# Kernel optimization log

Measured on AMD Instinct MI355X. Metric: run time of the kernel, lower is better.

The kernel has to match this reference:

```python
import jax, jax.numpy as jnp
import numpy as np

B, N, D_IN, D_OUT, NHOP = 16, 1024, 128, 128, 3


def setup_inputs() -> dict:
    key = jax.random.key(0)
    ks = jax.random.split(key, 7)
    x = jax.random.normal(ks[0], (B, N, D_IN), dtype=jnp.float32)
    # sparse-ish binary adjacency (float, as in the torch model) with self loops
    adj = (jax.random.uniform(ks[1], (B, N, N)) < 0.05).astype(jnp.float32)
    adj = jnp.maximum(adj, jnp.eye(N, dtype=jnp.float32)[None])
    # learned params (torch nn.Linear default-ish init scale)
    s_in = 1.0 / np.sqrt(D_IN)
    s_out = 1.0 / np.sqrt(2 * D_OUT)
    W_w = jax.random.uniform(ks[2], (D_OUT, D_IN), minval=-s_in, maxval=s_in, dtype=jnp.float32)
    W_b = jax.random.uniform(ks[3], (D_OUT,), minval=-s_in, maxval=s_in, dtype=jnp.float32)
    A = jax.random.normal(ks[4], (D_OUT, D_OUT), dtype=jnp.float32) * 0.02  # nn.Parameter(zeros) would kill signal; use small init
    gate_w = jax.random.uniform(ks[5], (1, 2 * D_OUT), minval=-s_out, maxval=s_out, dtype=jnp.float32)
    gate_b = jax.random.uniform(ks[6], (1,), minval=-s_out, maxval=s_out, dtype=jnp.float32)
    return {"x": x, "adj": adj, "W_w": W_w, "W_b": W_b, "A": A,
            "gate_w": gate_w, "gate_b": gate_b}


def reference(x, adj, W_w, W_b, A, gate_w, gate_b):
    # h = W(x): [B,N,D_OUT]
    h = jnp.einsum('bnd,od->bno', x, W_w) + W_b
    # bilinear score e[b,j,k] = (h A)_j . h_k, symmetrized
    e = jnp.einsum('bjl,bkl->bjk', jnp.einsum('bjd,de->bje', h, A), h)
    e = e + jnp.swapaxes(e, 1, 2)
    # masked softmax over dim=1 (as in the torch code), then re-mask
    att = jnp.where(adj > 0, e, jnp.zeros((), dtype=e.dtype))
    att = jax.nn.softmax(att, axis=1)
    att = att * adj
    retval = h
    for _ in range(NHOP):
        az = jax.nn.relu(jnp.einsum('bij,bjk->bik', att, retval))
        gate_in = jnp.concatenate([h, az], axis=-1)            # [B,N,2*D_OUT]
        coeff = jax.nn.sigmoid(jnp.einsum('bnf,of->bno', gate_in, gate_w) + gate_b)  # [B,N,1]
        retval = coeff * h + (1.0 - coeff) * az
    return retval
```

## Files before the change

kernel.cpp:

```cpp
#include <hip/hip_runtime.h>
#include <math.h>

#define Bn 16
#define Nn 1024
#define Dn 128

typedef unsigned short ushort;
typedef unsigned long long u64;
typedef short short8 __attribute__((ext_vector_type(8)));
typedef float f32x4 __attribute__((ext_vector_type(4)));
typedef ushort us8 __attribute__((ext_vector_type(8)));
typedef ushort us4 __attribute__((ext_vector_type(4)));

__device__ __forceinline__ ushort f2bf(float f) {
    unsigned u = __float_as_uint(f);
    u += 0x7fff + ((u >> 16) & 1);
    return (ushort)(u >> 16);
}
__device__ __forceinline__ float bf2f(ushort s) {
    return __uint_as_float(((unsigned)s) << 16);
}

#if defined(__has_builtin)
#if __has_builtin(__builtin_amdgcn_global_load_lds)
#define HAVE_GLL 1
#endif
#endif
#ifndef HAVE_GLL
#define HAVE_GLL 0
#endif

typedef __attribute__((address_space(1))) void as1_t;
typedef __attribute__((address_space(3))) void as3_t;

__device__ __forceinline__ void stage_group(const void* gbase, void* lbase, int lane) {
#if HAVE_GLL
    __builtin_amdgcn_global_load_lds((as1_t*)((const char*)gbase + lane * 16),
                                     (as3_t*)lbase, 16, 0, 0);
#else
    *(us8*)((char*)lbase + lane * 16) = *(const us8*)((const char*)gbase + lane * 16);
#endif
}


__global__ __launch_bounds__(256) void k_ph0(const float* __restrict__ Ww,
                                             const float* __restrict__ A,
                                             const float* __restrict__ adj,
                                             ushort* __restrict__ Whi, ushort* __restrict__ Wlo,
                                             ushort* __restrict__ Shi, ushort* __restrict__ Slo,
                                             float* __restrict__ Z, u64* __restrict__ bm) {
    int L = blockIdx.x, t = threadIdx.x;
    if (L < 64) {
        int i = L * 256 + t;
        float w = Ww[i];
        ushort wh = f2bf(w);
        Whi[i] = wh;
        Wlo[i] = f2bf(w - bf2f(wh));
        int e = i >> 7, d = i & 127;
        float s = A[i] + A[d * Dn + e];
        ushort sh = f2bf(s);
        Shi[i] = sh;
        Slo[i] = f2bf(s - bf2f(sh));
        Z[i] = (float)Nn;
    }
    int gwv = L * 4 + (t >> 6);
    int lane = t & 63;
    #pragma unroll 4
    for (int it = 0; it < 16; ++it) {
        int pair = gwv * 16 + it;
        const float* p = adj + (size_t)pair * 256 + lane * 4;
        float4 v = *(const float4*)p;
        u64 b0 = __ballot(v.x > 0.f);
        u64 b1 = __ballot(v.y > 0.f);
        u64 b2 = __ballot(v.z > 0.f);
        u64 b3 = __ballot(v.w > 0.f);
        if (lane == 0) {
            u64* d = bm + (size_t)pair * 4;
            d[0] = b0; d[1] = b1; d[2] = b2; d[3] = b3;
        }
    }
}

__global__ __launch_bounds__(256) void k_h(const float* __restrict__ x,
                                           const float* __restrict__ Wb,
                                           const ushort* __restrict__ Whi,
                                           const ushort* __restrict__ Wlo,
                                           const ushort* __restrict__ Shi,
                                           const ushort* __restrict__ Slo,
                                           float* __restrict__ h,
                                           ushort* __restrict__ h16f,
                                           ushort* __restrict__ g16f) {
    int I0 = blockIdx.x * 16;
    int t = threadIdx.x, w = t >> 6, lane = t & 63;
    int m = lane & 15, q = lane >> 4;

    __shared__ float xs[16][Dn + 4];
    __shared__ float hs[16][Dn + 4];
    __shared__ float gs_[16][Dn + 4];

    {
        int r = t >> 4, c8 = (t & 15) * 8;
        const float* src = x + (size_t)(I0 + r) * Dn + c8;
        *(float4*)&xs[r][c8]     = *(const float4*)(src);
        *(float4*)&xs[r][c8 + 4] = *(const float4*)(src + 4);
    }
    __syncthreads();

    f32x4 acc0 = {0,0,0,0}, acc1 = {0,0,0,0};
    #pragma unroll
    for (int ks = 0; ks < 4; ++ks) {
        int k0 = q * 8 + ks * 32;
        float v[8]; short8 ahi, alo;
        *(float4*)(v)     = *(const float4*)(&xs[m][k0]);
        *(float4*)(v + 4) = *(const float4*)(&xs[m][k0 + 4]);
        #pragma unroll
        for (int j = 0; j < 8; ++j) {
            ushort hi = f2bf(v[j]);
            ahi[j] = (short)hi;
            alo[j] = (short)f2bf(v[j] - bf2f(hi));
        }
        #pragma unroll
        for (int nn = 0; nn < 2; ++nn) {
            int brow = (w * 2 + nn) * 16 + m;
            short8 bhi = __builtin_bit_cast(short8, ((const us8*)(Whi + (size_t)brow * Dn))[q + ks * 4]);
            short8 blo = __builtin_bit_cast(short8, ((const us8*)(Wlo + (size_t)brow * Dn))[q + ks * 4]);
            f32x4 acc = nn ? acc1 : acc0;
            acc = __builtin_amdgcn_mfma_f32_16x16x32_bf16(ahi, bhi, acc, 0, 0, 0);
            acc = __builtin_amdgcn_mfma_f32_16x16x32_bf16(alo, bhi, acc, 0, 0, 0);
            acc = __builtin_amdgcn_mfma_f32_16x16x32_bf16(ahi, blo, acc, 0, 0, 0);
            if (nn) acc1 = acc; else acc0 = acc;
        }
    }
    #pragma unroll
    for (int nn = 0; nn < 2; ++nn) {
        int col = (w * 2 + nn) * 16 + m;
        float bias = Wb[col];
        f32x4 acc = nn ? acc1 : acc0;
        #pragma unroll
        for (int r = 0; r < 4; ++r) {
            int rl = q * 4 + r;
            float hv = acc[r] + bias;
            h[(size_t)(I0 + rl) * Dn + col] = hv;
            hs[rl][col] = hv;
        }
    }
    __syncthreads();

    f32x4 bcc0 = {0,0,0,0}, bcc1 = {0,0,0,0};
    #pragma unroll
    for (int ks = 0; ks < 4; ++ks) {
        int k0 = q * 8 + ks * 32;
        float v[8]; short8 ahi, alo;
        *(float4*)(v)     = *(const float4*)(&hs[m][k0]);
        *(float4*)(v + 4) = *(const float4*)(&hs[m][k0 + 4]);
        #pragma unroll
        for (int j = 0; j < 8; ++j) {
            ushort hi = f2bf(v[j]);
            ahi[j] = (short)hi;
            alo[j] = (short)f2bf(v[j] - bf2f(hi));
        }
        #pragma unroll
        for (int nn = 0; nn < 2; ++nn) {
            int brow = (w * 2 + nn) * 16 + m;
            short8 bhi = __builtin_bit_cast(short8, ((const us8*)(Shi + (size_t)brow * Dn))[q + ks * 4]);
            short8 blo = __builtin_bit_cast(short8, ((const us8*)(Slo + (size_t)brow * Dn))[q + ks * 4]);
            f32x4 acc = nn ? bcc1 : bcc0;
            acc = __builtin_amdgcn_mfma_f32_16x16x32_bf16(ahi, bhi, acc, 0, 0, 0);
            acc = __builtin_amdgcn_mfma_f32_16x16x32_bf16(alo, bhi, acc, 0, 0, 0);
            acc = __builtin_amdgcn_mfma_f32_16x16x32_bf16(ahi, blo, acc, 0, 0, 0);
            if (nn) bcc1 = acc; else bcc0 = acc;
        }
    }
    #pragma unroll
    for (int nn = 0; nn < 2; ++nn) {
        int col = (w * 2 + nn) * 16 + m;
        f32x4 acc = nn ? bcc1 : bcc0;
        #pragma unroll
        for (int r = 0; r < 4; ++r)
            gs_[q * 4 + r][col] = acc[r];
    }
    __syncthreads();

    {
        int kc = t >> 6, mm = (t >> 2) & 15, qq = t & 3;
        int cb = kc * 32 + qq * 8;
        us8 oh, oa;
        #pragma unroll
        for (int e = 0; e < 8; ++e) {
            oh[e] = f2bf(hs[mm][cb + e]);
            oa[e] = f2bf(gs_[mm][cb + e]);
        }
        size_t U = (size_t)(I0 >> 4) * 256 + kc * 64 + qq * 16 + mm;
        ((us8*)h16f)[U] = oh;
        ((us8*)g16f)[U] = oa;
    }
}

__global__ __launch_bounds__(256, 4) void k_scores(const ushort* __restrict__ g16f,
                                                   const ushort* __restrict__ h16f,
                                                   const u64* __restrict__ bm,
                                                   ushort* __restrict__ Ef,
                                                   float* __restrict__ Z) {
    int L = blockIdx.x;
    int b    = ((L & 7) << 1) | (L >> 11);
    int tile = (L >> 3) & 255;
    int I0 = (tile >> 4) << 6;
    int J0 = (tile & 15) << 6;
    int t = threadIdx.x, wid = t >> 6, lane = t & 63;
    int loff = lane * 16;

    __shared__ __align__(16) char smem[18432];
    float (*sc)[68] = (float(*)[68])smem;
    float (*cz)[64] = (float(*)[64])(smem + 17408);

    {
        const char* hbp = (const char*)h16f + (size_t)b * 262144;
        for (int g = wid; g < 16; g += 4) {
            int rt_l = g >> 2, kk = g & 3;
            stage_group(hbp + ((size_t)((J0 >> 4) + rt_l) * 256 + kk * 64) * 16,
                        smem + g * 1024, lane);
        }
    }
    short8 afr[4];
    {
        const char* gbp = (const char*)g16f + (size_t)b * 262144
                        + (size_t)((I0 >> 4) + wid) * 4096 + loff;
        #pragma unroll
        for (int ks = 0; ks < 4; ++ks)
            afr[ks] = __builtin_bit_cast(short8, *(const us8*)(gbp + ks * 1024));
    }
    __syncthreads();

    f32x4 acc[4] = {};
    #pragma unroll
    for (int ks = 0; ks < 4; ++ks) {
        #pragma unroll
        for (int nt = 0; nt < 4; ++nt) {
            short8 bb = __builtin_bit_cast(short8,
                *(const us8*)(smem + (nt * 4 + ks) * 1024 + loff));
            acc[nt] = __builtin_amdgcn_mfma_f32_16x16x32_bf16(afr[ks], bb, acc[nt], 0, 0, 0);
        }
    }
    __syncthreads();

    {
        int m = lane & 15, q = lane >> 4;
        #pragma unroll
        for (int nt = 0; nt < 4; ++nt)
            #pragma unroll
            for (int r = 0; r < 4; ++r)
                sc[wid * 16 + q * 4 + r][nt * 16 + m] = acc[nt][r];
    }
    __syncthreads();

    int row16 = t >> 4, c = t & 15;
    int bitc = ((J0 >> 2) & 63) + c;
    float colsum[4] = {0.f, 0.f, 0.f, 0.f};
    #pragma unroll
    for (int it = 0; it < 4; ++it) {
        int row = it * 16 + row16;
        const u64* wp = bm + ((size_t)(b * Nn + I0 + row) * 4 + (J0 >> 8)) * 4;
        u64 wj[4] = {wp[0], wp[1], wp[2], wp[3]};
        float s4[4];
        *(float4*)s4 = *(const float4*)(&sc[row][c * 4]);
        us4 e4;
        #pragma unroll
        for (int j = 0; j < 4; ++j) {
            float ex = __expf(s4[j]);
            bool on = (wj[j] >> bitc) & 1;
            e4[j] = f2bf(on ? ex : 0.f);
            colsum[j] += on ? (ex - 1.0f) : 0.f;
        }
        size_t base = ((((size_t)b * 64 + (I0 >> 4) + it) * 32 + (J0 >> 5) + (c >> 3)) * 512)
                    + (size_t)((c & 7) >> 1) * 128 + row16 * 8 + (c & 1) * 4;
        *(us4*)(Ef + base) = e4;
    }
    #pragma unroll
    for (int j = 0; j < 4; ++j) {
        colsum[j] += __shfl_xor(colsum[j], 16, 64);
        colsum[j] += __shfl_xor(colsum[j], 32, 64);
    }
    if (lane < 16) {
        #pragma unroll
        for (int j = 0; j < 4; ++j) cz[wid][lane * 4 + j] = colsum[j];
    }
    __syncthreads();
    if (t < 64) {
        float s = cz[0][t] + cz[1][t] + cz[2][t] + cz[3][t];
        atomicAdd(&Z[b * Nn + J0 + t], s);
    }
}

__global__ __launch_bounds__(256) void k_prep(const float* __restrict__ src,
                                              const float* __restrict__ Z,
                                              ushort* __restrict__ Tf) {
    int b = blockIdx.y;
    int j0 = blockIdx.x * 64;
    int t = threadIdx.x;
    __shared__ float ls[64][129];
    __shared__ float iz[64];
    if (t < 64) iz[t] = 1.0f / Z[b * Nn + j0 + t];
    __syncthreads();
    #pragma unroll
    for (int it = 0; it < 8; ++it) {
        int idx = it * 256 + t;
        int j = idx >> 5, k4 = (idx & 31) * 4;
        float4 v = *(const float4*)(src + ((size_t)b * Nn + j0 + j) * Dn + k4);
        float z = iz[j];
        ls[j][k4] = v.x * z; ls[j][k4 + 1] = v.y * z;
        ls[j][k4 + 2] = v.z * z; ls[j][k4 + 3] = v.w * z;
    }
    __syncthreads();
    int k = t & 127, half = t >> 7;
    us8 o[4];
    #pragma unroll
    for (int qq = 0; qq < 4; ++qq) {
        us8 tmp;
        #pragma unroll
        for (int e = 0; e < 8; ++e)
            tmp[e] = f2bf(ls[half * 32 + qq * 8 + e][k]);
        o[qq] = tmp;
    }
    size_t G = (size_t)(k >> 4) * 32 + (j0 >> 5) + half;
    ushort* dst = Tf + (size_t)b * 131072 + G * 512 + (size_t)(k & 15) * 8;
    #pragma unroll
    for (int qq = 0; qq < 4; ++qq)
        *(us8*)(dst + qq * 128) = o[qq];
}

#define STAGEB(BUF, cch) do {                                                          \
    for (int g = w; g < 32; g += 4)                                                    \
        stage_group(tfb + ((size_t)(g >> 2) * 32 + (cch) * 4 + (g & 3)) * 1024,        \
                    smem + (BUF) * 32768 + g * 1024, lane);                            \
} while (0)

#define ELOAD(SET, cch) do {                                                           \
    _Pragma("unroll")                                                                  \
    for (int kk = 0; kk < 4; ++kk)                                                     \
        SET[kk] = __builtin_bit_cast(short8,                                           \
            *(const us8*)(ebase + ((cch) * 4 + kk) * 1024));                           \
} while (0)

#define MFMAC(BUF, SET) do {                                                           \
    _Pragma("unroll")                                                                  \
    for (int kk = 0; kk < 4; ++kk) {                                                   \
        _Pragma("unroll")                                                              \
        for (int nt = 0; nt < 8; ++nt) {                                               \
            short8 bf = __builtin_bit_cast(short8,                                     \
                *(const us8*)(smem + (BUF) * 32768 + (nt * 4 + kk) * 1024 + loff));    \
            acc[nt] = __builtin_amdgcn_mfma_f32_16x16x32_bf16(SET[kk], bf, acc[nt], 0, 0, 0); \
        }                                                                              \
    }                                                                                  \
} while (0)

#define WAITB(NC) do {                                                                 \
    asm volatile("s_waitcnt vmcnt(" #NC ")" ::: "memory");                             \
    __builtin_amdgcn_s_barrier();                                                      \
} while (0)

__global__ __launch_bounds__(256, 1) void k_hop(const ushort* __restrict__ Ef,
                                                const ushort* __restrict__ Tf,
                                                const float* __restrict__ h,
                                                const float* __restrict__ Z,
                                                const float* __restrict__ gw,
                                                const float* __restrict__ gb,
                                                ushort* __restrict__ Tfn,
                                                float* __restrict__ out,
                                                int last) {
    int L = blockIdx.x;
    int b  = ((L & 7) << 1) | (L >> 7);
    int t4 = (L >> 3) & 15;
    int t = threadIdx.x, w = t >> 6, lane = t & 63;
    int m = lane & 15, q = lane >> 4;
    int rt = t4 * 4 + w;
    int I0 = rt << 4;
    int loff = lane * 16;

    __shared__ __align__(16) char smem[98304];
    const char* tfb   = (const char*)Tf + (size_t)b * 262144;
    const char* ebase = (const char*)Ef + (size_t)(b * 64 + rt) * 32768 + loff;

    f32x4 acc[8] = {};
    short8 aA[4], aB[4], aC[4];

    STAGEB(0, 0); ELOAD(aA, 0);
    STAGEB(1, 1); ELOAD(aB, 1);

    WAITB(16); STAGEB(2, 2); ELOAD(aC, 2); MFMAC(0, aA);
    WAITB(16); STAGEB(0, 3); ELOAD(aA, 3); MFMAC(1, aB);
    WAITB(16); STAGEB(1, 4); ELOAD(aB, 4); MFMAC(2, aC);
    WAITB(16); STAGEB(2, 5); ELOAD(aC, 5); MFMAC(0, aA);
    WAITB(16); STAGEB(0, 6); ELOAD(aA, 6); MFMAC(1, aB);
    WAITB(16); STAGEB(1, 7); ELOAD(aB, 7); MFMAC(2, aC);
    WAITB(16);                             MFMAC(0, aA);
    WAITB(4);                              MFMAC(1, aB);

    float gb0 = gb[0];
    float gwa[8], gwz[8];
    #pragma unroll
    for (int nt = 0; nt < 8; ++nt) { gwa[nt] = gw[nt * 16 + m]; gwz[nt] = gw[Dn + nt * 16 + m]; }

    float hv[8][4], coef[4];
    size_t hbase = ((size_t)b * Nn + I0) * Dn;
    #pragma unroll
    for (int r = 0; r < 4; ++r) {
        int row = q * 4 + r;
        float gs = 0.f;
        #pragma unroll
        for (int nt = 0; nt < 8; ++nt) {
            float az = fmaxf(acc[nt][r], 0.f);
            acc[nt][r] = az;
            float hh = h[hbase + (size_t)row * Dn + nt * 16 + m];
            hv[nt][r] = hh;
            gs += hh * gwa[nt] + az * gwz[nt];
        }
        gs += __shfl_xor(gs, 1, 64);
        gs += __shfl_xor(gs, 2, 64);
        gs += __shfl_xor(gs, 4, 64);
        gs += __shfl_xor(gs, 8, 64);
        coef[r] = 1.0f / (1.0f + __expf(-(gs + gb0)));
    }

    if (last) {
        #pragma unroll
        for (int r = 0; r < 4; ++r) {
            int row = q * 4 + r;
            float cc = coef[r];
            #pragma unroll
            for (int nt = 0; nt < 8; ++nt)
                out[hbase + (size_t)row * Dn + nt * 16 + m] =
                    cc * hv[nt][r] + (1.f - cc) * acc[nt][r];
        }
    } else {
        ushort (*tt)[128][16] = (ushort(*)[128][16])smem;
        #pragma unroll
        for (int r = 0; r < 4; ++r) {
            int row = q * 4 + r;
            float cc = coef[r];
            float iz = 1.0f / Z[b * Nn + I0 + row];
            #pragma unroll
            for (int nt = 0; nt < 8; ++nt) {
                float v = cc * hv[nt][r] + (1.f - cc) * acc[nt][r];
                tt[w][nt * 16 + m][row] = f2bf(v * iz);
            }
        }
        __syncthreads();
        int k = t >> 1, jh = t & 1;
        size_t G = (size_t)(k >> 4) * 32 + t4 * 2 + jh;
        ushort* dst = Tfn + (size_t)b * 131072 + G * 512 + (size_t)(k & 15) * 8;
        #pragma unroll
        for (int qq = 0; qq < 4; ++qq)
            *(us8*)(dst + qq * 128) = *(const us8*)&tt[jh * 2 + (qq >> 1)][k][(qq & 1) * 8];
    }
}

extern "C" void kernel_launch(void* const* d_in, const int* in_sizes, int n_in,
                              void* d_out, int out_size, void* d_ws, size_t ws_size,
                              hipStream_t stream) {
    const float* x    = (const float*)d_in[0];
    const float* adj  = (const float*)d_in[1];
    const float* Ww   = (const float*)d_in[2];
    const float* Wb   = (const float*)d_in[3];
    const float* A    = (const float*)d_in[4];
    const float* gw   = (const float*)d_in[5];
    const float* gb   = (const float*)d_in[6];
    float* out = (float*)d_out;

    char* ws = (char*)d_ws;
    float*  h    = (float*)(ws);
    ushort* Ta   = (ushort*)(ws + (8u << 20));
    ushort* Tb   = (ushort*)(ws + (12u << 20));
    ushort* E    = (ushort*)(ws + (16u << 20));
    float*  Z    = (float*)(ws + (48u << 20));
    ushort* Whi  = (ushort*)(ws + (48u << 20) + (64u << 10));
    ushort* Wlo  = (ushort*)(ws + (48u << 20) + (96u << 10));
    ushort* Shi  = (ushort*)(ws + (48u << 20) + (128u << 10));
    ushort* Slo  = (ushort*)(ws + (48u << 20) + (160u << 10));
    u64*    bm   = (u64*)(ws + (48u << 20) + (192u << 10));

    k_ph0   <<<1024, 256, 0, stream>>>(Ww, A, adj, Whi, Wlo, Shi, Slo, Z, bm);
    k_h     <<<1024, 256, 0, stream>>>(x, Wb, Whi, Wlo, Shi, Slo, h, Ta, Tb);
    k_scores<<<4096, 256, 0, stream>>>(Tb, Ta, bm, E, Z);
    k_prep  <<<dim3(16, Bn), 256, 0, stream>>>(h, Z, Ta);
    k_hop   <<<256, 256, 0, stream>>>(E, Ta, h, Z, gw, gb, Tb, out, 0);
    k_hop   <<<256, 256, 0, stream>>>(E, Tb, h, Z, gw, gb, Ta, out, 0);
    k_hop   <<<256, 256, 0, stream>>>(E, Ta, h, Z, gw, gb, (ushort*)nullptr, out, 1);
}
```

Baseline: 193.2 us.

## Split hop kernel output columns across two wave groups with 512 threads

The hop kernel moves from 256 to 512 threads per block. Each row tile is now handled by two waves, and each wave computes half of the 128 output columns, so per-wave MFMA work and accumulator registers are halved. The gate dot product becomes a partial sum per half, combined through shared memory with an added block barrier. Staging of the shared-memory buffers is spread across 8 waves, and the E-fragment loads are duplicated across the column halves, which adds global load traffic.

After: 192.1 us. No clear change (-0.5%).

```diff
diff --git a/kernel.cpp b/kernel.cpp
--- a/kernel.cpp
+++ b/kernel.cpp
@@ -329,7 +329,7 @@
 }
 
 #define STAGEB(BUF, cch) do {                                                          \
-    for (int g = w; g < 32; g += 4)                                                    \
+    for (int g = w; g < 32; g += 8)                                                    \
         stage_group(tfb + ((size_t)(g >> 2) * 32 + (cch) * 4 + (g & 3)) * 1024,        \
                     smem + (BUF) * 32768 + g * 1024, lane);                            \
 } while (0)
@@ -345,10 +345,10 @@
     _Pragma("unroll")                                                                  \
     for (int kk = 0; kk < 4; ++kk) {                                                   \
         _Pragma("unroll")                                                              \
-        for (int nt = 0; nt < 8; ++nt) {                                               \
+        for (int nt2 = 0; nt2 < 4; ++nt2) {                                            \
             short8 bf = __builtin_bit_cast(short8,                                     \
-                *(const us8*)(smem + (BUF) * 32768 + (nt * 4 + kk) * 1024 + loff));    \
-            acc[nt] = __builtin_amdgcn_mfma_f32_16x16x32_bf16(SET[kk], bf, acc[nt], 0, 0, 0); \
+                *(const us8*)(smem + (BUF) * 32768 + choff + (nt2 * 4 + kk) * 1024 + loff)); \
+            acc[nt2] = __builtin_amdgcn_mfma_f32_16x16x32_bf16(SET[kk], bf, acc[nt2], 0, 0, 0); \
         }                                                                              \
     }                                                                                  \
 } while (0)
@@ -358,7 +358,7 @@
     __builtin_amdgcn_s_barrier();                                                      \
 } while (0)
 
-__global__ __launch_bounds__(256, 1) void k_hop(const ushort* __restrict__ Ef,
+__global__ __launch_bounds__(512, 1) void k_hop(const ushort* __restrict__ Ef,
                                                 const ushort* __restrict__ Tf,
                                                 const float* __restrict__ h,
                                                 const float* __restrict__ Z,
@@ -372,53 +372,72 @@
     int t4 = (L >> 3) & 15;
     int t = threadIdx.x, w = t >> 6, lane = t & 63;
     int m = lane & 15, q = lane >> 4;
-    int rt = t4 * 4 + w;
+    int wr = w & 3, ch = w >> 2;
+    int rt = t4 * 4 + wr;
     int I0 = rt << 4;
     int loff = lane * 16;
+    int choff = ch * 16384;
 
     __shared__ __align__(16) char smem[98304];
+    __shared__ float gpart[4][16][2];
+
     const char* tfb   = (const char*)Tf + (size_t)b * 262144;
     const char* ebase = (const char*)Ef + (size_t)(b * 64 + rt) * 32768 + loff;
 
-    f32x4 acc[8] = {};
+    f32x4 acc[4] = {};
     short8 aA[4], aB[4], aC[4];
 
     STAGEB(0, 0); ELOAD(aA, 0);
     STAGEB(1, 1); ELOAD(aB, 1);
 
-    WAITB(16); STAGEB(2, 2); ELOAD(aC, 2); MFMAC(0, aA);
-    WAITB(16); STAGEB(0, 3); ELOAD(aA, 3); MFMAC(1, aB);
-    WAITB(16); STAGEB(1, 4); ELOAD(aB, 4); MFMAC(2, aC);
-    WAITB(16); STAGEB(2, 5); ELOAD(aC, 5); MFMAC(0, aA);
-    WAITB(16); STAGEB(0, 6); ELOAD(aA, 6); MFMAC(1, aB);
-    WAITB(16); STAGEB(1, 7); ELOAD(aB, 7); MFMAC(2, aC);
-    WAITB(16);                             MFMAC(0, aA);
-    WAITB(4);                              MFMAC(1, aB);
+    WAITB(8); STAGEB(2, 2); ELOAD(aC, 2); MFMAC(0, aA);
+    WAITB(8); STAGEB(0, 3); ELOAD(aA, 3); MFMAC(1, aB);
+    WAITB(8); STAGEB(1, 4); ELOAD(aB, 4); MFMAC(2, aC);
+    WAITB(8); STAGEB(2, 5); ELOAD(aC, 5); MFMAC(0, aA);
+    WAITB(8); STAGEB(0, 6); ELOAD(aA, 6); MFMAC(1, aB);
+    WAITB(8); STAGEB(1, 7); ELOAD(aB, 7); MFMAC(2, aC);
+    WAITB(8);                             MFMAC(0, aA);
+    WAITB(0);                             MFMAC(1, aB);
 
     float gb0 = gb[0];
-    float gwa[8], gwz[8];
-    #pragma unroll
-    for (int nt = 0; nt < 8; ++nt) { gwa[nt] = gw[nt * 16 + m]; gwz[nt] = gw[Dn + nt * 16 + m]; }
-
-    float hv[8][4], coef[4];
+    float gwa[4], gwz[4];
+    #pragma unroll
+    for (int nt2 = 0; nt2 < 4; ++nt2) {
+        gwa[nt2] = gw[ch * 64 + nt2 * 16 + m];
+        gwz[nt2] = gw[Dn + ch * 64 + nt2 * 16 + m];
+    }
+
+    float hv[4][4], gsr[4];
     size_t hbase = ((size_t)b * Nn + I0) * Dn;
     #pragma unroll
     for (int r = 0; r < 4; ++r) {
         int row = q * 4 + r;
         float gs = 0.f;
         #pragma unroll
-        for (int nt = 0; nt < 8; ++nt) {
-            float az = fmaxf(acc[nt][r], 0.f);
-            acc[nt][r] = az;
-            float hh = h[hbase + (size_t)row * Dn + nt * 16 + m];
-            hv[nt][r] = hh;
-            gs += hh * gwa[nt] + az * gwz[nt];
+        for (int nt2 = 0; nt2 < 4; ++nt2) {
+            float az = fmaxf(acc[nt2][r], 0.f);
+            acc[nt2][r] = az;
+            float hh = h[hbase + (size_t)row * Dn + ch * 64 + nt2 * 16 + m];
+            hv[nt2][r] = hh;
+            gs += hh * gwa[nt2] + az * gwz[nt2];
         }
         gs += __shfl_xor(gs, 1, 64);
         gs += __shfl_xor(gs, 2, 64);
         gs += __shfl_xor(gs, 4, 64);
         gs += __shfl_xor(gs, 8, 64);
-        coef[r] = 1.0f / (1.0f + __expf(-(gs + gb0)));
+        gsr[r] = gs;
+    }
+    if (m == 0) {
+        #pragma unroll
+        for (int r = 0; r < 4; ++r) gpart[wr][q * 4 + r][ch] = gsr[r];
+    }
+    __syncthreads();
+
+    float coef[4];
+    #pragma unroll
+    for (int r = 0; r < 4; ++r) {
+        float g2 = gpart[wr][q * 4 + r][0] + gpart[wr][q * 4 + r][1];
+        coef[r] = 1.0f / (1.0f + __expf(-(g2 + gb0)));
     }
 
     if (last) {
@@ -427,9 +446,9 @@
             int row = q * 4 + r;
             float cc = coef[r];
             #pragma unroll
-            for (int nt = 0; nt < 8; ++nt)
-                out[hbase + (size_t)row * Dn + nt * 16 + m] =
-                    cc * hv[nt][r] + (1.f - cc) * acc[nt][r];
+            for (int nt2 = 0; nt2 < 4; ++nt2)
+                out[hbase + (size_t)row * Dn + ch * 64 + nt2 * 16 + m] =
+                    cc * hv[nt2][r] + (1.f - cc) * acc[nt2][r];
         }
     } else {
         ushort (*tt)[128][16] = (ushort(*)[128][16])smem;
@@ -439,18 +458,20 @@
             float cc = coef[r];
             float iz = 1.0f / Z[b * Nn + I0 + row];
             #pragma unroll
-            for (int nt = 0; nt < 8; ++nt) {
-                float v = cc * hv[nt][r] + (1.f - cc) * acc[nt][r];
-                tt[w][nt * 16 + m][row] = f2bf(v * iz);
+            for (int nt2 = 0; nt2 < 4; ++nt2) {
+                float v = cc * hv[nt2][r] + (1.f - cc) * acc[nt2][r];
+                tt[wr][ch * 64 + nt2 * 16 + m][row] = f2bf(v * iz);
             }
         }
         __syncthreads();
-        int k = t >> 1, jh = t & 1;
-        size_t G = (size_t)(k >> 4) * 32 + t4 * 2 + jh;
-        ushort* dst = Tfn + (size_t)b * 131072 + G * 512 + (size_t)(k & 15) * 8;
-        #pragma unroll
-        for (int qq = 0; qq < 4; ++qq)
-            *(us8*)(dst + qq * 128) = *(const us8*)&tt[jh * 2 + (qq >> 1)][k][(qq & 1) * 8];
+        if (t < 256) {
+            int k = t >> 1, jh = t & 1;
+            size_t G = (size_t)(k >> 4) * 32 + t4 * 2 + jh;
+            ushort* dst = Tfn + (size_t)b * 131072 + G * 512 + (size_t)(k & 15) * 8;
+            #pragma unroll
+            for (int qq = 0; qq < 4; ++qq)
+                *(us8*)(dst + qq * 128) = *(const us8*)&tt[jh * 2 + (qq >> 1)][k][(qq & 1) * 8];
+        }
     }
 }
 
@@ -482,7 +503,7 @@
     k_h     <<<1024, 256, 0, stream>>>(x, Wb, Whi, Wlo, Shi, Slo, h, Ta, Tb);
     k_scores<<<4096, 256, 0, stream>>>(Tb, Ta, bm, E, Z);
     k_prep  <<<dim3(16, Bn), 256, 0, stream>>>(h, Z, Ta);
-    k_hop   <<<256, 256, 0, stream>>>(E, Ta, h, Z, gw, gb, Tb, out, 0);
-    k_hop   <<<256, 256, 0, stream>>>(E, Tb, h, Z, gw, gb, Ta, out, 0);
-    k_hop   <<<256, 256, 0, stream>>>(E, Ta, h, Z, gw, gb, (ushort*)nullptr, out, 1);
-}
+    k_hop   <<<256, 512, 0, stream>>>(E, Ta, h, Z, gw, gb, Tb, out, 0);
+    k_hop   <<<256, 512, 0, stream>>>(E, Tb, h, Z, gw, gb, Ta, out, 0);
+    k_hop   <<<256, 512, 0, stream>>>(E, Ta, h, Z, gw, gb, (ushort*)nullptr, out, 1);
+}
```

## Split hop kernel K-reduction across two wave groups with LDS combine

Applied to the files above, without the earlier changes.

The hop kernel now runs 512 threads per block. Two groups of four waves each take half of the j-reduction (4 of 8 chunks), each double-buffered in its own 64KB LDS region, and the partial accumulators are summed through shared memory before the gating epilogue. The h, gate weights and 1/Z loads are hoisted ahead of the main loop, and MFMA sections raise wave priority with s_setprio. The goal is more waves in flight per CU to hide the latency of the load-bound pipeline. The cost is extra LDS traffic and barriers for the combine step, plus half the threads sitting idle during the epilogue.

Measured after the change: 191.6 us. About the same (-0.8%).

```diff
diff --git a/kernel.cpp b/kernel.cpp
--- a/kernel.cpp
+++ b/kernel.cpp
@@ -328,29 +328,34 @@
         *(us8*)(dst + qq * 128) = o[qq];
 }
 
-#define STAGEB(BUF, cch) do {                                                          \
-    for (int g = w; g < 32; g += 4)                                                    \
-        stage_group(tfb + ((size_t)(g >> 2) * 32 + (cch) * 4 + (g & 3)) * 1024,        \
-                    smem + (BUF) * 32768 + g * 1024, lane);                            \
+#define SSTAGE(BUF, gc) do {                                                           \
+    _Pragma("unroll")                                                                  \
+    for (int j = 0; j < 8; ++j) {                                                      \
+        int g = rr * 8 + j;                         \
+        stage_group(tfb + ((size_t)(g >> 2) * 32 + (gc) * 4 + (g & 3)) * 1024,         \
+                    sbase + (BUF) * 32768 + g * 1024, lane);                           \
+    }                                                                                  \
 } while (0)
 
-#define ELOAD(SET, cch) do {                                                           \
+#define ELD(SET, gc) do {                                                              \
     _Pragma("unroll")                                                                  \
     for (int kk = 0; kk < 4; ++kk)                                                     \
         SET[kk] = __builtin_bit_cast(short8,                                           \
-            *(const us8*)(ebase + ((cch) * 4 + kk) * 1024));                           \
+            *(const us8*)(ebase + ((gc) * 4 + kk) * 1024));                            \
 } while (0)
 
-#define MFMAC(BUF, SET) do {                                                           \
+#define SMFMA(BUF, SET) do {                                                           \
+    __builtin_amdgcn_s_setprio(1);                                                     \
     _Pragma("unroll")                                                                  \
     for (int kk = 0; kk < 4; ++kk) {                                                   \
         _Pragma("unroll")                                                              \
         for (int nt = 0; nt < 8; ++nt) {                                               \
             short8 bf = __builtin_bit_cast(short8,                                     \
-                *(const us8*)(smem + (BUF) * 32768 + (nt * 4 + kk) * 1024 + loff));    \
+                *(const us8*)(sbase + (BUF) * 32768 + (nt * 4 + kk) * 1024 + loff));   \
             acc[nt] = __builtin_amdgcn_mfma_f32_16x16x32_bf16(SET[kk], bf, acc[nt], 0, 0, 0); \
         }                                                                              \
     }                                                                                  \
+    __builtin_amdgcn_s_setprio(0);                                                     \
 } while (0)
 
 #define WAITB(NC) do {                                                                 \
@@ -358,7 +363,7 @@
     __builtin_amdgcn_s_barrier();                                                      \
 } while (0)
 
-__global__ __launch_bounds__(256, 1) void k_hop(const ushort* __restrict__ Ef,
+__global__ __launch_bounds__(512, 1) void k_hop(const ushort* __restrict__ Ef,
                                                 const ushort* __restrict__ Tf,
                                                 const float* __restrict__ h,
                                                 const float* __restrict__ Z,
@@ -368,89 +373,120 @@
                                                 float* __restrict__ out,
                                                 int last) {
     int L = blockIdx.x;
-    int b  = ((L & 7) << 1) | (L >> 7);
-    int t4 = (L >> 3) & 15;
+    int b   = ((L & 7) << 1) | (L >> 7);
+    int rtp = (L >> 3) & 15;
     int t = threadIdx.x, w = t >> 6, lane = t & 63;
     int m = lane & 15, q = lane >> 4;
-    int rt = t4 * 4 + w;
+    int rr = w & 3, ks = w >> 2;
+    int rt = rtp * 4 + rr;
     int I0 = rt << 4;
     int loff = lane * 16;
 
-    __shared__ __align__(16) char smem[98304];
+    __shared__ __align__(16) char smem[131072];
+    char* sbase = smem + ks * 65536;
+
     const char* tfb   = (const char*)Tf + (size_t)b * 262144;
     const char* ebase = (const char*)Ef + (size_t)(b * 64 + rt) * 32768 + loff;
 
+    float hv[8][4], izr[4], gwa[8], gwz[8];
+    float gb0 = gb[0];
+    size_t hbase = ((size_t)b * Nn + I0) * Dn;
+    if (ks == 0) {
+        #pragma unroll
+        for (int r = 0; r < 4; ++r) izr[r] = 1.0f / Z[b * Nn + I0 + q * 4 + r];
+        #pragma unroll
+        for (int nt = 0; nt < 8; ++nt) {
+            gwa[nt] = gw[nt * 16 + m];
+            gwz[nt] = gw[Dn + nt * 16 + m];
+            #pragma unroll
+            for (int r = 0; r < 4; ++r)
+                hv[nt][r] = h[hbase + (size_t)(q * 4 + r) * Dn + nt * 16 + m];
+        }
+    }
+    asm volatile("s_waitcnt vmcnt(0)" ::: "memory");
+
+    int gc0 = ks * 4;
     f32x4 acc[8] = {};
-    short8 aA[4], aB[4], aC[4];
-
-    STAGEB(0, 0); ELOAD(aA, 0);
-    STAGEB(1, 1); ELOAD(aB, 1);
-
-    WAITB(16); STAGEB(2, 2); ELOAD(aC, 2); MFMAC(0, aA);
-    WAITB(16); STAGEB(0, 3); ELOAD(aA, 3); MFMAC(1, aB);
-    WAITB(16); STAGEB(1, 4); ELOAD(aB, 4); MFMAC(2, aC);
-    WAITB(16); STAGEB(2, 5); ELOAD(aC, 5); MFMAC(0, aA);
-    WAITB(16); STAGEB(0, 6); ELOAD(aA, 6); MFMAC(1, aB);
-    WAITB(16); STAGEB(1, 7); ELOAD(aB, 7); MFMAC(2, aC);
-    WAITB(16);                             MFMAC(0, aA);
-    WAITB(4);                              MFMAC(1, aB);
-
-    float gb0 = gb[0];
-    float gwa[8], gwz[8];
-    #pragma unroll
-    for (int nt = 0; nt < 8; ++nt) { gwa[nt] = gw[nt * 16 + m]; gwz[nt] = gw[Dn + nt * 16 + m]; }
-
-    float hv[8][4], coef[4];
-    size_t hbase = ((size_t)b * Nn + I0) * Dn;
-    #pragma unroll
-    for (int r = 0; r < 4; ++r) {
-        int row = q * 4 + r;
-        float gs = 0.f;
-        #pragma unroll
-        for (int nt = 0; nt < 8; ++nt) {
-            float az = fmaxf(acc[nt][r], 0.f);
-            acc[nt][r] = az;
-            float hh = h[hbase + (size_t)row * Dn + nt * 16 + m];
-            hv[nt][r] = hh;
-            gs += hh * gwa[nt] + az * gwz[nt];
-        }
-        gs += __shfl_xor(gs, 1, 64);
-        gs += __shfl_xor(gs, 2, 64);
-        gs += __shfl_xor(gs, 4, 64);
-        gs += __shfl_xor(gs, 8, 64);
-        coef[r] = 1.0f / (1.0f + __expf(-(gs + gb0)));
-    }
-
-    if (last) {
+    short8 eA[4], eB[4];
+
+    SSTAGE(0, gc0);     ELD(eA, gc0);
+    WAITB(4);
+    SSTAGE(1, gc0 + 1); ELD(eB, gc0 + 1); SMFMA(0, eA);
+    WAITB(4);
+    SSTAGE(0, gc0 + 2); ELD(eA, gc0 + 2); SMFMA(1, eB);
+    WAITB(4);
+    SSTAGE(1, gc0 + 3); ELD(eB, gc0 + 3); SMFMA(0, eA);
+    WAITB(4);
+                                          SMFMA(1, eB);
+    __syncthreads();
+
+    float (*cmb)[8][16][16] = (float(*)[8][16][16])(smem + 65536);
+    if (ks == 1) {
+        #pragma unroll
+        for (int nt = 0; nt < 8; ++nt)
+            #pragma unroll
+            for (int r = 0; r < 4; ++r)
+                cmb[rr][nt][q * 4 + r][m] = acc[nt][r];
+    }
+    __syncthreads();
+
+    ushort (*tt)[128][16] = (ushort(*)[128][16])smem;
+    if (ks == 0) {
+        #pragma unroll
+        for (int nt = 0; nt < 8; ++nt)
+            #pragma unroll
+            for (int r = 0; r < 4; ++r)
+                acc[nt][r] += cmb[rr][nt][q * 4 + r][m];
+
+        float coef[4];
         #pragma unroll
         for (int r = 0; r < 4; ++r) {
-            int row = q * 4 + r;
-            float cc = coef[r];
-            #pragma unroll
-            for (int nt = 0; nt < 8; ++nt)
-                out[hbase + (size_t)row * Dn + nt * 16 + m] =
-                    cc * hv[nt][r] + (1.f - cc) * acc[nt][r];
-        }
-    } else {
-        ushort (*tt)[128][16] = (ushort(*)[128][16])smem;
-        #pragma unroll
-        for (int r = 0; r < 4; ++r) {
-            int row = q * 4 + r;
-            float cc = coef[r];
-            float iz = 1.0f / Z[b * Nn + I0 + row];
+            float gs = 0.f;
             #pragma unroll
             for (int nt = 0; nt < 8; ++nt) {
-                float v = cc * hv[nt][r] + (1.f - cc) * acc[nt][r];
-                tt[w][nt * 16 + m][row] = f2bf(v * iz);
+                float az = fmaxf(acc[nt][r], 0.f);
+                acc[nt][r] = az;
+                gs += hv[nt][r] * gwa[nt] + az * gwz[nt];
             }
-        }
+            gs += __shfl_xor(gs, 1, 64);
+            gs += __shfl_xor(gs, 2, 64);
+            gs += __shfl_xor(gs, 4, 64);
+            gs += __shfl_xor(gs, 8, 64);
+            coef[r] = 1.0f / (1.0f + __expf(-(gs + gb0)));
+        }
+
+        if (last) {
+            #pragma unroll
+            for (int r = 0; r < 4; ++r) {
+                float cc = coef[r];
+                #pragma unroll
+                for (int nt = 0; nt < 8; ++nt)
+                    out[hbase + (size_t)(q * 4 + r) * Dn + nt * 16 + m] =
+                        cc * hv[nt][r] + (1.f - cc) * acc[nt][r];
+            }
+        } else {
+            #pragma unroll
+            for (int r = 0; r < 4; ++r) {
+                float cc = coef[r];
+                float iz = izr[r];
+                #pragma unroll
+                for (int nt = 0; nt < 8; ++nt) {
+                    float v = cc * hv[nt][r] + (1.f - cc) * acc[nt][r];
+                    tt[rr][nt * 16 + m][q * 4 + r] = f2bf(v * iz);
+                }
+            }
+        }
+    }
+    if (!last) {
         __syncthreads();
-        int k = t >> 1, jh = t & 1;
-        size_t G = (size_t)(k >> 4) * 32 + t4 * 2 + jh;
-        ushort* dst = Tfn + (size_t)b * 131072 + G * 512 + (size_t)(k & 15) * 8;
-        #pragma unroll
-        for (int qq = 0; qq < 4; ++qq)
-            *(us8*)(dst + qq * 128) = *(const us8*)&tt[jh * 2 + (qq >> 1)][k][(qq & 1) * 8];
+        if (t < 256) {
+            int k = t >> 1, jh = t & 1;
+            size_t G = (size_t)(k >> 4) * 32 + rtp * 2 + jh;
+            ushort* dst = Tfn + (size_t)b * 131072 + G * 512 + (size_t)(k & 15) * 8;
+            #pragma unroll
+            for (int qq = 0; qq < 4; ++qq)
+                *(us8*)(dst + qq * 128) = *(const us8*)&tt[jh * 2 + (qq >> 1)][k][(qq & 1) * 8];
+        }
     }
 }
 
@@ -482,7 +518,7 @@
     k_h     <<<1024, 256, 0, stream>>>(x, Wb, Whi, Wlo, Shi, Slo, h, Ta, Tb);
     k_scores<<<4096, 256, 0, stream>>>(Tb, Ta, bm, E, Z);
     k_prep  <<<dim3(16, Bn), 256, 0, stream>>>(h, Z, Ta);
-    k_hop   <<<256, 256, 0, stream>>>(E, Ta, h, Z, gw, gb, Tb, out, 0);
-    k_hop   <<<256, 256, 0, stream>>>(E, Tb, h, Z, gw, gb, Ta, out, 0);
-    k_hop   <<<256, 256, 0, stream>>>(E, Ta, h, Z, gw, gb, (ushort*)nullptr, out, 1);
-}
+    k_hop   <<<256, 512, 0, stream>>>(E, Ta, h, Z, gw, gb, Tb, out, 0);
+    k_hop   <<<256, 512, 0, stream>>>(E, Tb, h, Z, gw, gb, Ta, out, 0);
+    k_hop   <<<256, 512, 0, stream>>>(E, Ta, h, Z, gw, gb, (ushort*)nullptr, out, 1);
+}
```
